# Optimization experiments

Hardware: AMD Instinct MI355X
Metric: run time of the kernel (lower is better)

## Reference

```python
import jax, jax.numpy as jnp
import numpy as np

B, NI, H, NC = 524288, 32, 128, 64


def _masks(ni, h):
    deg_in = jnp.arange(ni)                     # input layer: arange % ni == arange
    deg_hid = jnp.arange(h) % (ni - 1)
    deg_out = jnp.arange(2 * ni) % ni - 1
    m1 = (deg_hid[:, None] >= deg_in[None, :]).astype(jnp.float32)   # [H, NI]
    m2 = (deg_hid[:, None] >= deg_hid[None, :]).astype(jnp.float32)  # [H, H]
    m3 = (deg_out[:, None] >= deg_hid[None, :]).astype(jnp.float32)  # [2NI, H]
    return m1, m2, m3


def setup_inputs() -> dict:
    key = jax.random.key(0)
    ks = jax.random.split(key, 9)
    s = 0.05
    return {
        "x": jax.random.normal(ks[0], (B, NI), jnp.float32),
        "cond": jax.random.normal(ks[1], (B, NC), jnp.float32),
        "W1": jax.random.normal(ks[2], (H, NI), jnp.float32) * s,
        "b1": jnp.zeros((H,), jnp.float32),
        "Wc": jax.random.normal(ks[3], (H, NC), jnp.float32) * s,
        "W2": jax.random.normal(ks[4], (H, H), jnp.float32) * s,
        "b2": jnp.zeros((H,), jnp.float32),
        "W3": jax.random.normal(ks[5], (2 * NI, H), jnp.float32) * s,
        "b3": jnp.zeros((2 * NI,), jnp.float32),
    }


def reference(x, cond, W1, b1, Wc, W2, b2, W3, b3):
    ni = x.shape[1]
    h_dim = W1.shape[0]
    m1, m2, m3 = _masks(ni, h_dim)
    # joiner: masked linear + conditioning linear (no bias on cond)
    h = x @ (W1 * m1).T + b1 + cond @ Wc.T            # [B, H]
    h = jax.nn.relu(h)
    h = jax.nn.relu(h @ (W2 * m2).T + b2)             # [B, H]
    o = h @ (W3 * m3).T + b3                          # [B, 2NI]
    m_, a = o[:, :ni], o[:, ni:]
    a = jnp.clip(a, -5.0, 5.0)
    u = (x - m_) * jnp.exp(-a)
    logdet = -jnp.sum(a, axis=-1, keepdims=True)
    return u, logdet
```

## Files before the change

### kernel.cpp

```cpp
#include <hip/hip_runtime.h>


#define B_ROWS 524288
#define NI 32
#define HD 128
#define NC 64

#define L2_BASE 24
#define L3_BASE 56
#define N_FRAGS 72

typedef _Float16 half8 __attribute__((ext_vector_type(8)));
typedef float f32x4 __attribute__((ext_vector_type(4)));

__device__ inline f32x4 relu4(f32x4 v) {
  v[0] = fmaxf(v[0], 0.f); v[1] = fmaxf(v[1], 0.f);
  v[2] = fmaxf(v[2], 0.f); v[3] = fmaxf(v[3], 0.f);
  return v;
}

__device__ inline half8 cvt8(f32x4 lo, f32x4 hi) {
  half8 h;
  h[0] = (_Float16)lo[0]; h[1] = (_Float16)lo[1];
  h[2] = (_Float16)lo[2]; h[3] = (_Float16)lo[3];
  h[4] = (_Float16)hi[0]; h[5] = (_Float16)hi[1];
  h[6] = (_Float16)hi[2]; h[7] = (_Float16)hi[3];
  return h;
}

__global__ void prep_weights(const float* __restrict__ W1, const float* __restrict__ Wc,
                             const float* __restrict__ W2, const float* __restrict__ W3,
                             _Float16* __restrict__ wf) {
  int tid = blockIdx.x * blockDim.x + threadIdx.x;
  if (tid >= N_FRAGS * 64) return;
  int frag = tid >> 6;
  int lane = tid & 63;
  int q = lane >> 4, c = lane & 15;
  int L, jt, kt;
  if (frag < L2_BASE)      { L = 0; jt = frag / 3;              kt = frag % 3; }
  else if (frag < L3_BASE) { L = 1; jt = (frag - L2_BASE) >> 2; kt = (frag - L2_BASE) & 3; }
  else                     { L = 2; jt = (frag - L3_BASE) >> 2; kt = (frag - L3_BASE) & 3; }
  int j = jt * 16 + c;
  half8 v;
#pragma unroll
  for (int e = 0; e < 8; ++e) {
    int k = kt * 32 + (e >> 2) * 16 + q * 4 + (e & 3);
    float w;
    if (L == 0) {
      if (k < NI) w = ((j % 31) >= k) ? W1[j * NI + k] : 0.f;
      else        w = Wc[j * NC + (k - NI)];
    } else if (L == 1) {
      w = ((j % 31) >= (k % 31)) ? W2[j * HD + k] : 0.f;
    } else {
      w = (((j % 32) - 1) >= (k % 31)) ? W3[j * HD + k] : 0.f;
    }
    v[e] = (_Float16)w;
  }
  *(half8*)(wf + (size_t)tid * 8) = v;
}

__global__ __launch_bounds__(256, 3) void made_fused(
    const float* __restrict__ x, const float* __restrict__ cond,
    const float* __restrict__ b1, const float* __restrict__ b2,
    const float* __restrict__ b3, const _Float16* __restrict__ wf,
    float* __restrict__ out) {
  const int tid  = threadIdx.x;
  const int lane = tid & 63;
  const int wid  = tid >> 6;
  const int q = lane >> 4, c = lane & 15;
  const long rowbase = ((long)blockIdx.x * 4 + wid) * 32;

  f32x4 xv[2][2], cv[2][4];
#pragma unroll
  for (int nt = 0; nt < 2; ++nt) {
    const f32x4* xr = (const f32x4*)(x    + (rowbase + nt * 16 + c) * NI);
    const f32x4* cr = (const f32x4*)(cond + (rowbase + nt * 16 + c) * NC);
    xv[nt][0] = xr[q];     xv[nt][1] = xr[4 + q];
    cv[nt][0] = cr[q];     cv[nt][1] = cr[4 + q];
    cv[nt][2] = cr[8 + q]; cv[nt][3] = cr[12 + q];
  }

  half8 bf[3][2];
#pragma unroll
  for (int nt = 0; nt < 2; ++nt) {
    bf[0][nt] = cvt8(xv[nt][0], xv[nt][1]);
    bf[1][nt] = cvt8(cv[nt][0], cv[nt][1]);
    bf[2][nt] = cvt8(cv[nt][2], cv[nt][3]);
  }

  f32x4 acc[4][2];
  half8 h1[4][2];
#pragma unroll
  for (int jh = 0; jh < 2; ++jh) {
#pragma unroll
    for (int j4 = 0; j4 < 4; ++j4) {
      f32x4 bv = *(const f32x4*)(b1 + (jh * 4 + j4) * 16 + q * 4);
      acc[j4][0] = bv; acc[j4][1] = bv;
    }
#pragma unroll
    for (int j4 = 0; j4 < 4; ++j4) {
      int jt = jh * 4 + j4;
#pragma unroll
      for (int kt = 0; kt < 3; ++kt) {
        half8 a = *(const half8*)(wf + (((jt * 3 + kt) * 64 + lane) << 3));
#pragma unroll
        for (int nt = 0; nt < 2; ++nt)
          acc[j4][nt] = __builtin_amdgcn_mfma_f32_16x16x32_f16(a, bf[kt][nt], acc[j4][nt], 0, 0, 0);
      }
    }
#pragma unroll
    for (int p = 0; p < 2; ++p)
#pragma unroll
      for (int nt = 0; nt < 2; ++nt)
        h1[jh * 2 + p][nt] = cvt8(relu4(acc[p * 2][nt]), relu4(acc[p * 2 + 1][nt]));
  }

  half8 h2[4][2];
#pragma unroll
  for (int jh = 0; jh < 2; ++jh) {
#pragma unroll
    for (int j4 = 0; j4 < 4; ++j4) {
      f32x4 bv = *(const f32x4*)(b2 + (jh * 4 + j4) * 16 + q * 4);
      acc[j4][0] = bv; acc[j4][1] = bv;
    }
#pragma unroll
    for (int j4 = 0; j4 < 4; ++j4) {
      int jt = jh * 4 + j4;
#pragma unroll
      for (int kt = 0; kt < 4; ++kt) {
        half8 a = *(const half8*)(wf + (((L2_BASE + jt * 4 + kt) * 64 + lane) << 3));
#pragma unroll
        for (int nt = 0; nt < 2; ++nt)
          acc[j4][nt] = __builtin_amdgcn_mfma_f32_16x16x32_f16(a, h1[kt][nt], acc[j4][nt], 0, 0, 0);
      }
    }
#pragma unroll
    for (int p = 0; p < 2; ++p)
#pragma unroll
      for (int nt = 0; nt < 2; ++nt)
        h2[jh * 2 + p][nt] = cvt8(relu4(acc[p * 2][nt]), relu4(acc[p * 2 + 1][nt]));
  }

#pragma unroll
  for (int jt = 0; jt < 4; ++jt) {
    f32x4 bv = *(const f32x4*)(b3 + jt * 16 + q * 4);
    acc[jt][0] = bv; acc[jt][1] = bv;
  }
#pragma unroll
  for (int jt = 0; jt < 4; ++jt)
#pragma unroll
    for (int kt = 0; kt < 4; ++kt) {
      half8 a = *(const half8*)(wf + (((L3_BASE + jt * 4 + kt) * 64 + lane) << 3));
#pragma unroll
      for (int nt = 0; nt < 2; ++nt)
        acc[jt][nt] = __builtin_amdgcn_mfma_f32_16x16x32_f16(a, h2[kt][nt], acc[jt][nt], 0, 0, 0);
    }

#pragma unroll
  for (int nt = 0; nt < 2; ++nt) {
    long m = rowbase + nt * 16 + c;
    f32x4 xa = xv[nt][0], xb = xv[nt][1];
    f32x4 mva = acc[0][nt], mvb = acc[1][nt];
    f32x4 ava = acc[2][nt], avb = acc[3][nt];
    f32x4 ua, ub;
    float s = 0.f;
#pragma unroll
    for (int i = 0; i < 4; ++i) {
      float aa = fminf(fmaxf(ava[i], -5.f), 5.f);
      float ab = fminf(fmaxf(avb[i], -5.f), 5.f);
      ua[i] = (xa[i] - mva[i]) * __expf(-aa);
      ub[i] = (xb[i] - mvb[i]) * __expf(-ab);
      s += aa + ab;
    }
    *(f32x4*)(out + m * NI + q * 4) = ua;
    *(f32x4*)(out + m * NI + 16 + q * 4) = ub;
    s += __shfl_xor(s, 16);
    s += __shfl_xor(s, 32);
    if (q == 0) out[(long)B_ROWS * NI + m] = -s;
  }
}

extern "C" void kernel_launch(void* const* d_in, const int* in_sizes, int n_in,
                              void* d_out, int out_size, void* d_ws, size_t ws_size,
                              hipStream_t stream) {
  const float* x    = (const float*)d_in[0];
  const float* cond = (const float*)d_in[1];
  const float* W1   = (const float*)d_in[2];
  const float* b1   = (const float*)d_in[3];
  const float* Wc   = (const float*)d_in[4];
  const float* W2   = (const float*)d_in[5];
  const float* b2   = (const float*)d_in[6];
  const float* W3   = (const float*)d_in[7];
  const float* b3   = (const float*)d_in[8];
  _Float16* wf = (_Float16*)d_ws;

  prep_weights<<<(N_FRAGS * 64 + 255) / 256, 256, 0, stream>>>(W1, Wc, W2, W3, wf);
  made_fused<<<B_ROWS / 128, 256, 0, stream>>>(x, cond, b1, b2, b3, wf, (float*)d_out);
}
```

Baseline: 336.5 us.

## Switch to 32x32x16 MFMA tiles and stage layer-2 weights in LDS

Reworks the fused MADE kernel to use 32x32x16 f16 MFMA instead of 16x16x32, re-laying out the prepared weight fragments and the per-lane input, activation and output mapping to match. Layer-2 weights are copied asynchronously into shared memory with global_load_lds while layer 1 runs, and are then read from LDS. The aim is fewer MFMA issues and fewer global weight loads per wave. The cost is 32 KB of LDS per block, which may limit occupancy, plus a block-wide sync.

```diff
diff --git a/kernel.cpp b/kernel.cpp
--- a/kernel.cpp
+++ b/kernel.cpp
@@ -12,6 +12,7 @@
 
 typedef _Float16 half8 __attribute__((ext_vector_type(8)));
 typedef float f32x4 __attribute__((ext_vector_type(4)));
+typedef float f32x16 __attribute__((ext_vector_type(16)));
 
 __device__ inline f32x4 relu4(f32x4 v) {
   v[0] = fmaxf(v[0], 0.f); v[1] = fmaxf(v[1], 0.f);
@@ -28,6 +29,27 @@
   return h;
 }
 
+#define CVTQ2(D0, D1, A) do {                                                 \
+    f32x4 t0, t1, t2, t3;                                                     \
+    t0[0]=A[0]; t0[1]=A[1]; t0[2]=A[2]; t0[3]=A[3];                           \
+    t1[0]=A[4]; t1[1]=A[5]; t1[2]=A[6]; t1[3]=A[7];                           \
+    t2[0]=A[8]; t2[1]=A[9]; t2[2]=A[10]; t2[3]=A[11];                         \
+    t3[0]=A[12]; t3[1]=A[13]; t3[2]=A[14]; t3[3]=A[15];                       \
+    D0 = cvt8(relu4(t0), relu4(t1));                                          \
+    D1 = cvt8(relu4(t2), relu4(t3));                                          \
+  } while (0)
+
+#define BIAS16(A, BP, BASE) do {                                              \
+    f32x4 q0 = *(const f32x4*)((BP) + (BASE) + 4 * hh);                       \
+    f32x4 q1 = *(const f32x4*)((BP) + (BASE) + 4 * hh + 8);                   \
+    f32x4 q2 = *(const f32x4*)((BP) + (BASE) + 4 * hh + 16);                  \
+    f32x4 q3 = *(const f32x4*)((BP) + (BASE) + 4 * hh + 24);                  \
+    A[0]=q0[0]; A[1]=q0[1]; A[2]=q0[2]; A[3]=q0[3];                           \
+    A[4]=q1[0]; A[5]=q1[1]; A[6]=q1[2]; A[7]=q1[3];                           \
+    A[8]=q2[0]; A[9]=q2[1]; A[10]=q2[2]; A[11]=q2[3];                         \
+    A[12]=q3[0]; A[13]=q3[1]; A[14]=q3[2]; A[15]=q3[3];                       \
+  } while (0)
+
 __global__ void prep_weights(const float* __restrict__ W1, const float* __restrict__ Wc,
                              const float* __restrict__ W2, const float* __restrict__ W3,
                              _Float16* __restrict__ wf) {
@@ -35,16 +57,16 @@
   if (tid >= N_FRAGS * 64) return;
   int frag = tid >> 6;
   int lane = tid & 63;
-  int q = lane >> 4, c = lane & 15;
+  int hh = lane >> 5, nn = lane & 31;
   int L, jt, kt;
-  if (frag < L2_BASE)      { L = 0; jt = frag / 3;              kt = frag % 3; }
-  else if (frag < L3_BASE) { L = 1; jt = (frag - L2_BASE) >> 2; kt = (frag - L2_BASE) & 3; }
-  else                     { L = 2; jt = (frag - L3_BASE) >> 2; kt = (frag - L3_BASE) & 3; }
-  int j = jt * 16 + c;
+  if (frag < L2_BASE)      { L = 0; jt = frag / 6;              kt = frag % 6; }
+  else if (frag < L3_BASE) { L = 1; jt = (frag - L2_BASE) >> 3; kt = (frag - L2_BASE) & 7; }
+  else                     { L = 2; jt = (frag - L3_BASE) >> 3; kt = (frag - L3_BASE) & 7; }
+  int j = jt * 32 + nn;
   half8 v;
 #pragma unroll
   for (int e = 0; e < 8; ++e) {
-    int k = kt * 32 + (e >> 2) * 16 + q * 4 + (e & 3);
+    int k = kt * 16 + hh * 4 + (e & 3) + 8 * (e >> 2);
     float w;
     if (L == 0) {
       if (k < NI) w = ((j % 31) >= k) ? W1[j * NI + k] : 0.f;
@@ -64,120 +86,99 @@
     const float* __restrict__ b1, const float* __restrict__ b2,
     const float* __restrict__ b3, const _Float16* __restrict__ wf,
     float* __restrict__ out) {
+  __shared__ __align__(16) _Float16 wlds[32 * 512];
+
   const int tid  = threadIdx.x;
   const int lane = tid & 63;
   const int wid  = tid >> 6;
-  const int q = lane >> 4, c = lane & 15;
-  const long rowbase = ((long)blockIdx.x * 4 + wid) * 32;
-
-  f32x4 xv[2][2], cv[2][4];
-#pragma unroll
-  for (int nt = 0; nt < 2; ++nt) {
-    const f32x4* xr = (const f32x4*)(x    + (rowbase + nt * 16 + c) * NI);
-    const f32x4* cr = (const f32x4*)(cond + (rowbase + nt * 16 + c) * NC);
-    xv[nt][0] = xr[q];     xv[nt][1] = xr[4 + q];
-    cv[nt][0] = cr[q];     cv[nt][1] = cr[4 + q];
-    cv[nt][2] = cr[8 + q]; cv[nt][3] = cr[12 + q];
-  }
-
-  half8 bf[3][2];
-#pragma unroll
-  for (int nt = 0; nt < 2; ++nt) {
-    bf[0][nt] = cvt8(xv[nt][0], xv[nt][1]);
-    bf[1][nt] = cvt8(cv[nt][0], cv[nt][1]);
-    bf[2][nt] = cvt8(cv[nt][2], cv[nt][3]);
-  }
-
-  f32x4 acc[4][2];
-  half8 h1[4][2];
-#pragma unroll
-  for (int jh = 0; jh < 2; ++jh) {
-#pragma unroll
-    for (int j4 = 0; j4 < 4; ++j4) {
-      f32x4 bv = *(const f32x4*)(b1 + (jh * 4 + j4) * 16 + q * 4);
-      acc[j4][0] = bv; acc[j4][1] = bv;
-    }
-#pragma unroll
-    for (int j4 = 0; j4 < 4; ++j4) {
-      int jt = jh * 4 + j4;
-#pragma unroll
-      for (int kt = 0; kt < 3; ++kt) {
-        half8 a = *(const half8*)(wf + (((jt * 3 + kt) * 64 + lane) << 3));
-#pragma unroll
-        for (int nt = 0; nt < 2; ++nt)
-          acc[j4][nt] = __builtin_amdgcn_mfma_f32_16x16x32_f16(a, bf[kt][nt], acc[j4][nt], 0, 0, 0);
-      }
-    }
-#pragma unroll
-    for (int p = 0; p < 2; ++p)
-#pragma unroll
-      for (int nt = 0; nt < 2; ++nt)
-        h1[jh * 2 + p][nt] = cvt8(relu4(acc[p * 2][nt]), relu4(acc[p * 2 + 1][nt]));
-  }
-
-  half8 h2[4][2];
-#pragma unroll
-  for (int jh = 0; jh < 2; ++jh) {
-#pragma unroll
-    for (int j4 = 0; j4 < 4; ++j4) {
-      f32x4 bv = *(const f32x4*)(b2 + (jh * 4 + j4) * 16 + q * 4);
-      acc[j4][0] = bv; acc[j4][1] = bv;
-    }
-#pragma unroll
-    for (int j4 = 0; j4 < 4; ++j4) {
-      int jt = jh * 4 + j4;
-#pragma unroll
-      for (int kt = 0; kt < 4; ++kt) {
-        half8 a = *(const half8*)(wf + (((L2_BASE + jt * 4 + kt) * 64 + lane) << 3));
-#pragma unroll
-        for (int nt = 0; nt < 2; ++nt)
-          acc[j4][nt] = __builtin_amdgcn_mfma_f32_16x16x32_f16(a, h1[kt][nt], acc[j4][nt], 0, 0, 0);
-      }
-    }
-#pragma unroll
-    for (int p = 0; p < 2; ++p)
-#pragma unroll
-      for (int nt = 0; nt < 2; ++nt)
-        h2[jh * 2 + p][nt] = cvt8(relu4(acc[p * 2][nt]), relu4(acc[p * 2 + 1][nt]));
-  }
-
-#pragma unroll
-  for (int jt = 0; jt < 4; ++jt) {
-    f32x4 bv = *(const f32x4*)(b3 + jt * 16 + q * 4);
-    acc[jt][0] = bv; acc[jt][1] = bv;
-  }
-#pragma unroll
-  for (int jt = 0; jt < 4; ++jt)
-#pragma unroll
-    for (int kt = 0; kt < 4; ++kt) {
-      half8 a = *(const half8*)(wf + (((L3_BASE + jt * 4 + kt) * 64 + lane) << 3));
-#pragma unroll
-      for (int nt = 0; nt < 2; ++nt)
-        acc[jt][nt] = __builtin_amdgcn_mfma_f32_16x16x32_f16(a, h2[kt][nt], acc[jt][nt], 0, 0, 0);
-    }
-
-#pragma unroll
-  for (int nt = 0; nt < 2; ++nt) {
-    long m = rowbase + nt * 16 + c;
-    f32x4 xa = xv[nt][0], xb = xv[nt][1];
-    f32x4 mva = acc[0][nt], mvb = acc[1][nt];
-    f32x4 ava = acc[2][nt], avb = acc[3][nt];
-    f32x4 ua, ub;
-    float s = 0.f;
+  const int hh = lane >> 5, nn = lane & 31;
+  const long r = ((long)blockIdx.x * 4 + wid) * 32 + nn;
+
+  const f32x4* xr = (const f32x4*)(x + r * NI);
+  const f32x4* cr = (const f32x4*)(cond + r * NC);
+  f32x4 xv0 = xr[hh],     xv1 = xr[2 + hh], xv2 = xr[4 + hh], xv3 = xr[6 + hh];
+  f32x4 cv0 = cr[hh],     cv1 = cr[2 + hh], cv2 = cr[4 + hh], cv3 = cr[6 + hh];
+  f32x4 cv4 = cr[8 + hh], cv5 = cr[10 + hh], cv6 = cr[12 + hh], cv7 = cr[14 + hh];
+
+  {
+    const char* gsrc = (const char*)wf + L2_BASE * 1024 + wid * 8192;
+    char* ldst = (char*)wlds + wid * 8192;
+#pragma unroll
+    for (int i = 0; i < 8; ++i) {
+      __builtin_amdgcn_global_load_lds(
+          (const __attribute__((address_space(1))) void*)(gsrc + i * 1024 + lane * 16),
+          (__attribute__((address_space(3))) void*)(ldst + i * 1024),
+          16, 0, 0);
+    }
+  }
+
+  half8 bf[6];
+  bf[0] = cvt8(xv0, xv1); bf[1] = cvt8(xv2, xv3);
+  bf[2] = cvt8(cv0, cv1); bf[3] = cvt8(cv2, cv3);
+  bf[4] = cvt8(cv4, cv5); bf[5] = cvt8(cv6, cv7);
+
+  half8 hf1[8];
+#pragma unroll
+  for (int p = 0; p < 2; ++p) {
+    f32x16 A0, A1;
+    BIAS16(A0, b1, (2 * p) * 32);
+    BIAS16(A1, b1, (2 * p + 1) * 32);
+#pragma unroll
+    for (int kt = 0; kt < 6; ++kt) {
+      half8 w0 = *(const half8*)(wf + ((((2 * p) * 6 + kt) * 64 + lane) << 3));
+      half8 w1 = *(const half8*)(wf + ((((2 * p + 1) * 6 + kt) * 64 + lane) << 3));
+      A0 = __builtin_amdgcn_mfma_f32_32x32x16_f16(w0, bf[kt], A0, 0, 0, 0);
+      A1 = __builtin_amdgcn_mfma_f32_32x32x16_f16(w1, bf[kt], A1, 0, 0, 0);
+    }
+    CVTQ2(hf1[4 * p + 0], hf1[4 * p + 1], A0);
+    CVTQ2(hf1[4 * p + 2], hf1[4 * p + 3], A1);
+  }
+
+  __syncthreads();
+
+  half8 hf2[8];
+#pragma unroll
+  for (int p = 0; p < 2; ++p) {
+    f32x16 A0, A1;
+    BIAS16(A0, b2, (2 * p) * 32);
+    BIAS16(A1, b2, (2 * p + 1) * 32);
+#pragma unroll
+    for (int kt = 0; kt < 8; ++kt) {
+      half8 w0 = *(const half8*)(wlds + ((((2 * p) * 8 + kt) * 64 + lane) << 3));
+      half8 w1 = *(const half8*)(wlds + ((((2 * p + 1) * 8 + kt) * 64 + lane) << 3));
+      A0 = __builtin_amdgcn_mfma_f32_32x32x16_f16(w0, hf1[kt], A0, 0, 0, 0);
+      A1 = __builtin_amdgcn_mfma_f32_32x32x16_f16(w1, hf1[kt], A1, 0, 0, 0);
+    }
+    CVTQ2(hf2[4 * p + 0], hf2[4 * p + 1], A0);
+    CVTQ2(hf2[4 * p + 2], hf2[4 * p + 3], A1);
+  }
+
+  f32x16 Am, Aa;
+  BIAS16(Am, b3, 0);
+  BIAS16(Aa, b3, 32);
+#pragma unroll
+  for (int kt = 0; kt < 8; ++kt) {
+    half8 wm = *(const half8*)(wf + (((56 + kt) * 64 + lane) << 3));
+    half8 wa = *(const half8*)(wf + (((64 + kt) * 64 + lane) << 3));
+    Am = __builtin_amdgcn_mfma_f32_32x32x16_f16(wm, hf2[kt], Am, 0, 0, 0);
+    Aa = __builtin_amdgcn_mfma_f32_32x32x16_f16(wa, hf2[kt], Aa, 0, 0, 0);
+  }
+
+  float s = 0.f;
+#pragma unroll
+  for (int g = 0; g < 4; ++g) {
+    f32x4 xg = (g == 0) ? xv0 : (g == 1) ? xv1 : (g == 2) ? xv2 : xv3;
+    f32x4 u;
 #pragma unroll
     for (int i = 0; i < 4; ++i) {
-      float aa = fminf(fmaxf(ava[i], -5.f), 5.f);
-      float ab = fminf(fmaxf(avb[i], -5.f), 5.f);
-      ua[i] = (xa[i] - mva[i]) * __expf(-aa);
-      ub[i] = (xb[i] - mvb[i]) * __expf(-ab);
-      s += aa + ab;
-    }
-    *(f32x4*)(out + m * NI + q * 4) = ua;
-    *(f32x4*)(out + m * NI + 16 + q * 4) = ub;
-    s += __shfl_xor(s, 16);
-    s += __shfl_xor(s, 32);
-    if (q == 0) out[(long)B_ROWS * NI + m] = -s;
-  }
+      float aa = fminf(fmaxf(Aa[4 * g + i], -5.f), 5.f);
+      u[i] = (xg[i] - Am[4 * g + i]) * __expf(-aa);
+      s += aa;
+    }
+    *(f32x4*)(out + r * NI + 4 * hh + 8 * g) = u;
+  }
+  s += __shfl_xor(s, 32);
+  if (hh == 0) out[(long)B_ROWS * NI + r] = -s;
 }
 
 extern "C" void kernel_launch(void* const* d_in, const int* in_sizes, int n_in,
```

New measurement: 300.7 us. 1.12x faster.
